# Optimization experiments

Hardware: AMD Instinct MI355X
Metric: run time of the kernel (lower is better)

Reference implementation:

```python
import jax, jax.numpy as jnp
import numpy as np

B = 128
K = 16
# (in_ch, featdim, dim) per stage, matching conv1..conv11
DIMS = [(3, 8, 2048), (8, 32, 1024), (32, 64, 512), (64, 64, 256), (64, 64, 128),
        (64, 128, 64), (128, 256, 32), (256, 512, 16), (512, 512, 8), (512, 512, 4),
        (512, 1024, 2)]


def setup_inputs() -> dict:
    key = jax.random.key(0)
    ks = jax.random.split(key, 64)
    inp = {"x": jax.random.normal(ks[0], (B, 3, 2048), dtype=jnp.float32)}
    i = 1
    for li, (cin, cf, d) in enumerate(DIMS, start=1):
        inp[f"W{li}"] = jax.random.normal(ks[i], (3 * cf, cin), dtype=jnp.float32) / np.sqrt(cin).astype(np.float32); i += 1
        inp[f"b{li}"] = jax.random.normal(ks[i], (3 * cf,), dtype=jnp.float32) * 0.01; i += 1
        inp[f"sel{li}"] = jax.random.randint(ks[i], (d,), 0, 3); i += 1
    inp["fcW"] = jax.random.normal(ks[i], (K, 1024), dtype=jnp.float32) / np.sqrt(1024).astype(np.float32); i += 1
    inp["fcb"] = jax.random.normal(ks[i], (K,), dtype=jnp.float32) * 0.01
    return inp


def kdconv(x, W, b, sel, featdim, dim):
    # 1x1 conv == per-position matmul: x [B, Cin, dim] -> y [B, 3*featdim, dim]
    y = jax.nn.relu(jnp.einsum('oi,bin->bon', W, x) + b[None, :, None])
    y = y.reshape(-1, featdim, 3, dim)
    # kd split-dim gather: pick one of the 3 feature groups per position
    y = jnp.take_along_axis(y, sel[None, None, None, :], axis=2)[:, :, 0, :]  # [B, featdim, dim]
    # pairwise max-pool of sibling leaves
    return y.reshape(-1, featdim, dim // 2, 2).max(axis=-1)  # [B, featdim, dim//2]


def reference(x, sel1, sel2, sel3, sel4, sel5, sel6, sel7, sel8, sel9, sel10, sel11,
              W1, b1, W2, b2, W3, b3, W4, b4, W5, b5, W6, b6, W7, b7, W8, b8,
              W9, b9, W10, b10, W11, b11, fcW, fcb):
    Ws = [W1, W2, W3, W4, W5, W6, W7, W8, W9, W10, W11]
    bs = [b1, b2, b3, b4, b5, b6, b7, b8, b9, b10, b11]
    sels = [sel1, sel2, sel3, sel4, sel5, sel6, sel7, sel8, sel9, sel10, sel11]
    h = x
    for (cin, cf, d), W, b, s in zip(DIMS, Ws, bs, sels):
        h = kdconv(h, W, b, s, cf, d)
    h = h.reshape(-1, 1024)  # [B, 1024]
    return jax.nn.log_softmax(h @ fcW.T + fcb, axis=-1)
```

## Files before the change

kernel.cpp:

```cpp
#include <hip/hip_runtime.h>
#include <math.h>

typedef __attribute__((ext_vector_type(8))) short bf16x8;
typedef __attribute__((ext_vector_type(4))) float f32x4;

__device__ __forceinline__ unsigned short f2bf(float f) {
    unsigned u = __builtin_bit_cast(unsigned, f);
    u += 0x7FFF + ((u >> 16) & 1);
    return (unsigned short)(u >> 16);
}
__device__ __forceinline__ float bf2f(unsigned short h) {
    unsigned u = ((unsigned)h) << 16;
    return __builtin_bit_cast(float, u);
}

#define O_W8 153600
#define O_W9 546816
#define O_W10 1333248
#define O_W11 2119680

__device__ __forceinline__ bf16x8 ldcvt8(const float* p) {
    float4 u0 = *(const float4*)p;
    float4 u1 = *(const float4*)(p + 4);
    bf16x8 r;
    r[0] = (short)f2bf(u0.x); r[1] = (short)f2bf(u0.y);
    r[2] = (short)f2bf(u0.z); r[3] = (short)f2bf(u0.w);
    r[4] = (short)f2bf(u1.x); r[5] = (short)f2bf(u1.y);
    r[6] = (short)f2bf(u1.z); r[7] = (short)f2bf(u1.w);
    return r;
}

template<int CIN>
__device__ __forceinline__ void mfma_tile_f32A(
    const float* a0f, const float* a1f,
    const unsigned short* b0p, const unsigned short* b1p,
    f32x4& acc0, f32x4& acc1)
{
#pragma unroll
    for (int k = 0; k < CIN; k += 32) {
        bf16x8 A0 = ldcvt8(a0f + k);
        bf16x8 A1 = ldcvt8(a1f + k);
        bf16x8 B0 = __builtin_bit_cast(bf16x8, *(const float4*)(const void*)(b0p + k));
        bf16x8 B1 = __builtin_bit_cast(bf16x8, *(const float4*)(const void*)(b1p + k));
        acc0 = __builtin_amdgcn_mfma_f32_16x16x32_bf16(A0, B0, acc0, 0, 0, 0);
        acc1 = __builtin_amdgcn_mfma_f32_16x16x32_bf16(A1, B1, acc1, 0, 0, 0);
    }
}

__device__ __forceinline__ void epilogue_store(
    unsigned short* dst, const f32x4& acc0, const f32x4& acc1,
    const float* bias, int fbase, int s0, int s1)
{
    unsigned short o[4];
#pragma unroll
    for (int r = 0; r < 4; ++r) {
        float v = fmaxf(fmaxf(acc0[r] + bias[(fbase + r) * 3 + s0],
                              acc1[r] + bias[(fbase + r) * 3 + s1]), 0.f);
        o[r] = f2bf(v);
    }
    *(ushort4*)dst = make_ushort4(o[0], o[1], o[2], o[3]);
}

struct FusedParams {
    const float* x;
    const float* W1; const float* B1; const int* S1;
    const float* W2; const float* B2; const int* S2;
    const float* Wsrc[9];
    const float* Bl[9];
    const int*   Sl[9];
    unsigned short* Wb;
    unsigned short* X8;
};

#define A_SELB 0
#define A_XS   8192
#define A_L1O  33536
#define A_WSM  49920
#define A_L2O  53760
#define A_L3O  8192
#define A_L4O  53760
#define A_L5O  8192
#define A_L6O  53760
#define ARENA_BYTES 94720

__global__ __launch_bounds__(1024) void fused17_kernel(FusedParams P)
{
    const int tid = threadIdx.x;

    if (blockIdx.x >= 128) {
        int gt = (blockIdx.x - 128) * 1024 + tid;
        const int we[4] = {393216, 786432, 786432, 1572864};
        const int wo[4] = {O_W8, O_W9, O_W10, O_W11};
#pragma unroll
        for (int li = 0; li < 4; ++li) {
            const float4* src = (const float4*)P.Wsrc[5 + li];
            ushort4* dst = (ushort4*)(P.Wb + wo[li]);
            int n4 = we[li] >> 2;
            for (int i = gt; i < n4; i += 65536) {
                float4 w = src[i];
                dst[i] = make_ushort4(f2bf(w.x), f2bf(w.y), f2bf(w.z), f2bf(w.w));
            }
        }
        return;
    }

    __shared__ __align__(16) char arena[ARENA_BYTES];

    const int bg   = blockIdx.x >> 4;
    const int sl   = blockIdx.x & 15;
    const int lane = tid & 63;
    const int wv   = tid >> 6;
    const int c    = lane & 15, q = lane >> 4;

    int*   si  = (int*)(arena + A_SELB);
    float* bfs = (float*)(arena + A_SELB + 1024);
    const int* S1L = si;
    const int* S2L = si + 128;
    const int* S3L = si + 192;
    const int* S4L = si + 224;
    const int* S5L = si + 240;
    const int* S6L = si + 248;
    const int* S7L = si + 252;
    const float* B3L = bfs;
    const float* B4L = bfs + 192;
    const float* B5L = bfs + 384;
    const float* B6L = bfs + 576;
    const float* B7L = bfs + 960;

    {
        float* xsf = (float*)(arena + A_XS);
        const float* xg = P.x + (size_t)(bg * 16) * 6144 + sl * 128;
        for (int i = tid; i < 6144; i += 1024) {
            int b = i / 384;
            int r = i - b * 384;
            int cc = r >> 7, p = r & 127;
            xsf[b * 396 + cc * 132 + p] = xg[(size_t)b * 6144 + cc * 2048 + p];
        }
        float* wsm = (float*)(arena + A_WSM);
        if (tid < 960) {
            float v;
            if (tid < 72)       v = P.W1[tid];
            else if (tid < 96)  v = P.B1[tid - 72];
            else if (tid < 864) v = P.W2[tid - 96];
            else                v = P.B2[tid - 864];
            wsm[tid] = v;
        }
        if (tid < 128)      si[tid] = P.S1[sl * 128 + tid];
        else if (tid < 192) si[tid] = P.S2[sl * 64 + (tid - 128)];
        else if (tid < 224) si[tid] = P.Sl[0][sl * 32 + (tid - 192)];
        else if (tid < 240) si[tid] = P.Sl[1][sl * 16 + (tid - 224)];
        else if (tid < 248) si[tid] = P.Sl[2][sl * 8  + (tid - 240)];
        else if (tid < 252) si[tid] = P.Sl[3][sl * 4  + (tid - 248)];
        else if (tid < 254) si[tid] = P.Sl[4][sl * 2  + (tid - 252)];
        for (int i = tid; i < 1728; i += 1024) {
            float v;
            if (i < 192)      v = P.Bl[0][i];
            else if (i < 384) v = P.Bl[1][i - 192];
            else if (i < 576) v = P.Bl[2][i - 384];
            else if (i < 960) v = P.Bl[3][i - 576];
            else              v = P.Bl[4][i - 960];
            bfs[i] = v;
        }
    }
    __syncthreads();

    {
        const float* xsf = (const float*)(arena + A_XS);
        const float* wl1 = (const float*)(arena + A_WSM);
        const float* bl1 = wl1 + 72;
        unsigned short* L1o = (unsigned short*)(arena + A_L1O);
        int n = tid >> 4, b = tid & 15;
        int s0 = S1L[2 * n], s1 = S1L[2 * n + 1];
        const float* xb0 = xsf + b * 396 + 2 * n;
        float c0x = xb0[0],   c0y = xb0[1];
        float c1x = xb0[132], c1y = xb0[133];
        float c2x = xb0[264], c2y = xb0[265];
        unsigned short o[8];
#pragma unroll
        for (int f = 0; f < 8; ++f) {
            int r0 = f * 3 + s0, r1 = f * 3 + s1;
            float z0 = fmaf(wl1[r0*3+2], c2x, fmaf(wl1[r0*3+1], c1x, fmaf(wl1[r0*3+0], c0x, bl1[r0])));
            float z1 = fmaf(wl1[r1*3+2], c2y, fmaf(wl1[r1*3+1], c1y, fmaf(wl1[r1*3+0], c0y, bl1[r1])));
            o[f] = f2bf(fmaxf(fmaxf(z0, z1), 0.f));
        }
        unsigned short* dst = L1o + (n * 16 + b) * 8;
        *(ushort4*)dst       = make_ushort4(o[0], o[1], o[2], o[3]);
        *(ushort4*)(dst + 4) = make_ushort4(o[4], o[5], o[6], o[7]);
    }
    __syncthreads();

    {
        const float* wl2 = (const float*)(arena + A_WSM) + 96;
        const float* bl2 = (const float*)(arena + A_WSM) + 864;
        const unsigned short* L1o = (const unsigned short*)(arena + A_L1O);
        unsigned short* L2o = (unsigned short*)(arena + A_L2O);
        int n = tid >> 5, b = (tid >> 1) & 15, fh = tid & 1;
        int s0 = S2L[2 * n], s1 = S2L[2 * n + 1];
        const unsigned short* r0 = L1o + ((2 * n) * 16 + b) * 8;
        const unsigned short* r1 = L1o + ((2 * n + 1) * 16 + b) * 8;
        float xa[8], xb2[8];
        {
            ushort4 u0 = *(const ushort4*)r0, u1 = *(const ushort4*)(r0 + 4);
            ushort4 v0 = *(const ushort4*)r1, v1 = *(const ushort4*)(r1 + 4);
            xa[0]=bf2f(u0.x); xa[1]=bf2f(u0.y); xa[2]=bf2f(u0.z); xa[3]=bf2f(u0.w);
            xa[4]=bf2f(u1.x); xa[5]=bf2f(u1.y); xa[6]=bf2f(u1.z); xa[7]=bf2f(u1.w);
            xb2[0]=bf2f(v0.x); xb2[1]=bf2f(v0.y); xb2[2]=bf2f(v0.z); xb2[3]=bf2f(v0.w);
            xb2[4]=bf2f(v1.x); xb2[5]=bf2f(v1.y); xb2[6]=bf2f(v1.z); xb2[7]=bf2f(v1.w);
        }
        unsigned short o[16];
#pragma unroll
        for (int fl = 0; fl < 16; ++fl) {
            int f = fh * 16 + fl;
            const float* w0 = &wl2[(f * 3 + s0) * 8];
            const float* w1 = &wl2[(f * 3 + s1) * 8];
            float z0 = bl2[f * 3 + s0], z1 = bl2[f * 3 + s1];
#pragma unroll
            for (int k = 0; k < 8; ++k) {
                z0 = fmaf(w0[k], xa[k], z0);
                z1 = fmaf(w1[k], xb2[k], z1);
            }
            o[fl] = f2bf(fmaxf(fmaxf(z0, z1), 0.f));
        }
        unsigned short* dst = L2o + (n * 16 + b) * 40 + fh * 16;
#pragma unroll
        for (int i2 = 0; i2 < 4; ++i2)
            *(ushort4*)(dst + 4 * i2) = make_ushort4(o[4*i2], o[4*i2+1], o[4*i2+2], o[4*i2+3]);
    }
    __syncthreads();

    {
        const unsigned short* L2o = (const unsigned short*)(arena + A_L2O);
        unsigned short* L3o = (unsigned short*)(arena + A_L3O);
        const float* W3f = P.Wsrc[0];
#pragma unroll 2
        for (int t = wv; t < 64; t += 16) {
            int n3 = t >> 2, ft = t & 3;
            int s0 = __builtin_amdgcn_readfirstlane(S3L[2 * n3]);
            int s1 = __builtin_amdgcn_readfirstlane(S3L[2 * n3 + 1]);
            int f0 = ft * 16;
            const float* a0f = W3f + ((f0 + c) * 3 + s0) * 32 + q * 8;
            const float* a1f = W3f + ((f0 + c) * 3 + s1) * 32 + q * 8;
            const unsigned short* bp0 = L2o + ((2 * n3) * 16 + c) * 40 + q * 8;
            const unsigned short* bp1 = L2o + ((2 * n3 + 1) * 16 + c) * 40 + q * 8;
            f32x4 acc0 = {0.f,0.f,0.f,0.f}, acc1 = {0.f,0.f,0.f,0.f};
            mfma_tile_f32A<32>(a0f, a1f, bp0, bp1, acc0, acc1);
            epilogue_store(L3o + (n3 * 16 + c) * 72 + f0 + q * 4,
                           acc0, acc1, B3L, f0 + q * 4, s0, s1);
        }
    }
    __syncthreads();

    {
        const unsigned short* L3o = (const unsigned short*)(arena + A_L3O);
        unsigned short* L4o = (unsigned short*)(arena + A_L4O);
        const float* W4f = P.Wsrc[1];
#pragma unroll
        for (int t = wv; t < 32; t += 16) {
            int n4 = t >> 2, ft = t & 3;
            int s0 = __builtin_amdgcn_readfirstlane(S4L[2 * n4]);
            int s1 = __builtin_amdgcn_readfirstlane(S4L[2 * n4 + 1]);
            int f0 = ft * 16;
            const float* a0f = W4f + ((f0 + c) * 3 + s0) * 64 + q * 8;
            const float* a1f = W4f + ((f0 + c) * 3 + s1) * 64 + q * 8;
            const unsigned short* bp0 = L3o + ((2 * n4) * 16 + c) * 72 + q * 8;
            const unsigned short* bp1 = L3o + ((2 * n4 + 1) * 16 + c) * 72 + q * 8;
            f32x4 acc0 = {0.f,0.f,0.f,0.f}, acc1 = {0.f,0.f,0.f,0.f};
            mfma_tile_f32A<64>(a0f, a1f, bp0, bp1, acc0, acc1);
            epilogue_store(L4o + (n4 * 16 + c) * 72 + f0 + q * 4,
                           acc0, acc1, B4L, f0 + q * 4, s0, s1);
        }
    }
    __syncthreads();

    {
        const unsigned short* L4o = (const unsigned short*)(arena + A_L4O);
        unsigned short* L5o = (unsigned short*)(arena + A_L5O);
        const float* W5f = P.Wsrc[2];
        int t = wv;
        int n5 = t >> 2, ft = t & 3;
        int s0 = __builtin_amdgcn_readfirstlane(S5L[2 * n5]);
        int s1 = __builtin_amdgcn_readfirstlane(S5L[2 * n5 + 1]);
        int f0 = ft * 16;
        const float* a0f = W5f + ((f0 + c) * 3 + s0) * 64 + q * 8;
        const float* a1f = W5f + ((f0 + c) * 3 + s1) * 64 + q * 8;
        const unsigned short* bp0 = L4o + ((2 * n5) * 16 + c) * 72 + q * 8;
        const unsigned short* bp1 = L4o + ((2 * n5 + 1) * 16 + c) * 72 + q * 8;
        f32x4 acc0 = {0.f,0.f,0.f,0.f}, acc1 = {0.f,0.f,0.f,0.f};
        mfma_tile_f32A<64>(a0f, a1f, bp0, bp1, acc0, acc1);
        epilogue_store(L5o + (n5 * 16 + c) * 72 + f0 + q * 4,
                       acc0, acc1, B5L, f0 + q * 4, s0, s1);
    }
    __syncthreads();

    {
        const unsigned short* L5o = (const unsigned short*)(arena + A_L5O);
        unsigned short* L6o = (unsigned short*)(arena + A_L6O);
        const float* W6f = P.Wsrc[3];
        int t = wv;
        int n6 = t >> 3, ft = t & 7;
        int s0 = __builtin_amdgcn_readfirstlane(S6L[2 * n6]);
        int s1 = __builtin_amdgcn_readfirstlane(S6L[2 * n6 + 1]);
        int f0 = ft * 16;
        const float* a0f = W6f + ((f0 + c) * 3 + s0) * 64 + q * 8;
        const float* a1f = W6f + ((f0 + c) * 3 + s1) * 64 + q * 8;
        const unsigned short* bp0 = L5o + ((2 * n6) * 16 + c) * 72 + q * 8;
        const unsigned short* bp1 = L5o + ((2 * n6 + 1) * 16 + c) * 72 + q * 8;
        f32x4 acc0 = {0.f,0.f,0.f,0.f}, acc1 = {0.f,0.f,0.f,0.f};
        mfma_tile_f32A<64>(a0f, a1f, bp0, bp1, acc0, acc1);
        epilogue_store(L6o + (n6 * 16 + c) * 136 + f0 + q * 4,
                       acc0, acc1, B6L, f0 + q * 4, s0, s1);
    }
    __syncthreads();

    {
        const unsigned short* L6o = (const unsigned short*)(arena + A_L6O);
        const float* W7f = P.Wsrc[4];
        int s0 = __builtin_amdgcn_readfirstlane(S7L[0]);
        int s1 = __builtin_amdgcn_readfirstlane(S7L[1]);
        int f0 = wv * 16;
        const float* a0f = W7f + (size_t)((f0 + c) * 3 + s0) * 128 + q * 8;
        const float* a1f = W7f + (size_t)((f0 + c) * 3 + s1) * 128 + q * 8;
        const unsigned short* bp0 = L6o + (0 * 16 + c) * 136 + q * 8;
        const unsigned short* bp1 = L6o + (1 * 16 + c) * 136 + q * 8;
        f32x4 acc0 = {0.f,0.f,0.f,0.f}, acc1 = {0.f,0.f,0.f,0.f};
        mfma_tile_f32A<128>(a0f, a1f, bp0, bp1, acc0, acc1);
        epilogue_store(P.X8 + ((size_t)sl * 128 + bg * 16 + c) * 256 + f0 + q * 4,
                       acc0, acc1, B7L, f0 + q * 4, s0, s1);
    }
}

template<int CIN, int CF, int NP, int MW, int NW>
__global__ __launch_bounds__(256) void mfma_kernel(
    const unsigned short* __restrict__ Xin,
    const unsigned short* __restrict__ Wb,
    const float* __restrict__ bias,
    const int*   __restrict__ sel,
    unsigned short* __restrict__ Xout)
{
    constexpr int FT = CF / (16 * MW);
    constexpr int BT = 128 / (16 * NW);

    const int wid  = threadIdx.x >> 6;
    const int lane = threadIdx.x & 63;
    const int task = blockIdx.x * 4 + wid;
    const int bi = task % BT;
    const int fi = (task / BT) % FT;
    const int n  = task / (BT * FT);

    const int c = lane & 15;
    const int q = lane >> 4;
    const int s0 = __builtin_amdgcn_readfirstlane(sel[2 * n]);
    const int s1 = __builtin_amdgcn_readfirstlane(sel[2 * n + 1]);

    const int f0 = fi * 16 * MW;
    const int b0 = bi * 16 * NW;

    const unsigned short* ap[2][MW];
    const unsigned short* bp[2][NW];
#pragma unroll
    for (int p = 0; p < 2; ++p) {
        int s = p ? s1 : s0;
#pragma unroll
        for (int mi = 0; mi < MW; ++mi)
            ap[p][mi] = Wb + (size_t)((f0 + mi * 16 + c) * 3 + s) * CIN + q * 8;
#pragma unroll
        for (int ni = 0; ni < NW; ++ni)
            bp[p][ni] = Xin + ((size_t)(2 * n + p) * 128 + b0 + ni * 16 + c) * CIN + q * 8;
    }

    f32x4 acc[2][MW][NW];
#pragma unroll
    for (int p = 0; p < 2; ++p)
#pragma unroll
        for (int mi = 0; mi < MW; ++mi)
#pragma unroll
            for (int ni = 0; ni < NW; ++ni)
                acc[p][mi][ni] = (f32x4){0.f, 0.f, 0.f, 0.f};

#pragma unroll 2
    for (int k = 0; k < CIN; k += 32) {
        bf16x8 A[2][MW], B[2][NW];
#pragma unroll
        for (int p = 0; p < 2; ++p) {
#pragma unroll
            for (int mi = 0; mi < MW; ++mi)
                A[p][mi] = __builtin_bit_cast(bf16x8, *(const float4*)(const void*)(ap[p][mi] + k));
#pragma unroll
            for (int ni = 0; ni < NW; ++ni)
                B[p][ni] = __builtin_bit_cast(bf16x8, *(const float4*)(const void*)(bp[p][ni] + k));
        }
#pragma unroll
        for (int p = 0; p < 2; ++p)
#pragma unroll
            for (int mi = 0; mi < MW; ++mi)
#pragma unroll
                for (int ni = 0; ni < NW; ++ni)
                    acc[p][mi][ni] = __builtin_amdgcn_mfma_f32_16x16x32_bf16(
                        A[p][mi], B[p][ni], acc[p][mi][ni], 0, 0, 0);
    }

#pragma unroll
    for (int mi = 0; mi < MW; ++mi) {
        int fbase = f0 + mi * 16 + q * 4;
#pragma unroll
        for (int ni = 0; ni < NW; ++ni) {
            int b = b0 + ni * 16 + c;
            epilogue_store(Xout + ((size_t)n * 128 + b) * CF + fbase,
                           acc[0][mi][ni], acc[1][mi][ni], bias, fbase, s0, s1);
        }
    }
}

__global__ __launch_bounds__(256) void fc_logsoftmax_kernel(
    const unsigned short* __restrict__ h, const float* __restrict__ fcW,
    const float* __restrict__ fcb, float* __restrict__ out)
{
    int b   = blockIdx.x;
    int tid = threadIdx.x;
    int k     = tid & 15;
    int chunk = tid >> 4;

    const float* __restrict__ wk = fcW + (size_t)k * 1024;
    const unsigned short* hb = h + (size_t)b * 1024;

    float partial = 0.0f;
    int j0 = chunk * 64;
#pragma unroll 8
    for (int j = 0; j < 64; ++j)
        partial = fmaf(bf2f(hb[j0 + j]), wk[j0 + j], partial);

    __shared__ float red[16][17];
    red[chunk][k] = partial;
    __syncthreads();

    __shared__ float logits[16];
    if (tid < 16) {
        float s = fcb[tid];
#pragma unroll
        for (int c = 0; c < 16; ++c) s += red[c][tid];
        logits[tid] = s;
    }
    __syncthreads();

    if (tid < 16) {
        float mx = -INFINITY;
#pragma unroll
        for (int kk = 0; kk < 16; ++kk) mx = fmaxf(mx, logits[kk]);
        float se = 0.0f;
#pragma unroll
        for (int kk = 0; kk < 16; ++kk) se += expf(logits[kk] - mx);
        out[b * 16 + tid] = logits[tid] - mx - logf(se);
    }
}

extern "C" void kernel_launch(void* const* d_in, const int* in_sizes, int n_in,
                              void* d_out, int out_size, void* d_ws, size_t ws_size,
                              hipStream_t stream)
{
#define WL(i) (const float*)d_in[1 + 3 * (i)]
#define BL(i) (const float*)d_in[2 + 3 * (i)]
#define SL(i) (const int*)  d_in[3 + 3 * (i)]

    unsigned short* bufA = (unsigned short*)d_ws;
    unsigned short* bufB = bufA + 2u * 1024u * 1024u;
    unsigned short* Wb   = bufB + 2u * 1024u * 1024u;

    FusedParams FP;
    FP.x  = (const float*)d_in[0];
    FP.W1 = WL(0); FP.B1 = BL(0); FP.S1 = SL(0);
    FP.W2 = WL(1); FP.B2 = BL(1); FP.S2 = SL(1);
    for (int i = 0; i < 9; ++i) {
        FP.Wsrc[i] = WL(2 + i);
        FP.Bl[i]   = BL(2 + i);
        FP.Sl[i]   = SL(2 + i);
    }
    FP.Wb = Wb; FP.X8 = bufA;
    fused17_kernel<<<192, 1024, 0, stream>>>(FP);

    mfma_kernel<256, 512, 8, 2, 2><<<128, 256, 0, stream>>>(bufA, Wb + O_W8,  BL(7),  SL(7),  bufB);
    mfma_kernel<512, 512, 4, 1, 1><<<256, 256, 0, stream>>>(bufB, Wb + O_W9,  BL(8),  SL(8),  bufA);
    mfma_kernel<512, 512, 2, 1, 1><<<128, 256, 0, stream>>>(bufA, Wb + O_W10, BL(9),  SL(9),  bufB);
    mfma_kernel<512, 1024, 1, 1, 1><<<128, 256, 0, stream>>>(bufB, Wb + O_W11, BL(10), SL(10), bufA);

    fc_logsoftmax_kernel<<<128, 256, 0, stream>>>(bufA, (const float*)d_in[34], (const float*)d_in[35], (float*)d_out);

#undef WL
#undef BL
#undef SL
}
```

Baseline: 215.0 us.

## Split fused layer 1-7 kernel into L1-2 kernel and L3-7 kernel

The single 1024-thread fused kernel for layers 1-7 is split in two. A 256-thread kernel computes layers 1-2 and packs weights, then writes the layer-2 activations to a global buffer X3. A 512-thread kernel with a smaller shared arena then runs layers 3-7 and reads its input from X3. The aim is to cut per-block shared memory and thread count so occupancy and scheduling improve, at the cost of an extra launch and a global round trip for the layer-2 activations.

New measurement: 220.8 us. 2.7% more time.

```diff
diff --git a/kernel.cpp b/kernel.cpp
--- a/kernel.cpp
+++ b/kernel.cpp
@@ -61,34 +61,21 @@
     *(ushort4*)dst = make_ushort4(o[0], o[1], o[2], o[3]);
 }
 
-struct FusedParams {
+struct KAParams {
     const float* x;
     const float* W1; const float* B1; const int* S1;
     const float* W2; const float* B2; const int* S2;
     const float* Wsrc[9];
-    const float* Bl[9];
-    const int*   Sl[9];
     unsigned short* Wb;
-    unsigned short* X8;
+    unsigned short* X3;
 };
 
-#define A_SELB 0
-#define A_XS   8192
-#define A_L1O  33536
-#define A_WSM  49920
-#define A_L2O  53760
-#define A_L3O  8192
-#define A_L4O  53760
-#define A_L5O  8192
-#define A_L6O  53760
-#define ARENA_BYTES 94720
-
-__global__ __launch_bounds__(1024) void fused17_kernel(FusedParams P)
+__global__ __launch_bounds__(256) void ka_l12_pack(KAParams P)
 {
     const int tid = threadIdx.x;
 
     if (blockIdx.x >= 128) {
-        int gt = (blockIdx.x - 128) * 1024 + tid;
+        int gt = (blockIdx.x - 128) * 256 + tid;
         const int we[4] = {393216, 786432, 786432, 1572864};
         const int wo[4] = {O_W8, O_W9, O_W10, O_W11};
 #pragma unroll
@@ -96,7 +83,7 @@
             const float4* src = (const float4*)P.Wsrc[5 + li];
             ushort4* dst = (ushort4*)(P.Wb + wo[li]);
             int n4 = we[li] >> 2;
-            for (int i = gt; i < n4; i += 65536) {
+            for (int i = gt; i < n4; i += 32768) {
                 float4 w = src[i];
                 dst[i] = make_ushort4(f2bf(w.x), f2bf(w.y), f2bf(w.z), f2bf(w.w));
             }
@@ -104,144 +91,163 @@
         return;
     }
 
-    __shared__ __align__(16) char arena[ARENA_BYTES];
-
+    __shared__ __align__(16) float xsf[16 * 396];
+    __shared__ float wsm[960];
+    __shared__ unsigned short L1o[64 * 16 * 8];
+    __shared__ int selA[192];
+
+    const int bg = blockIdx.x >> 4;
+    const int sl = blockIdx.x & 15;
+
+    {
+        const float* xg = P.x + (size_t)(bg * 16) * 6144 + sl * 128;
+        for (int i = tid; i < 6144; i += 256) {
+            int b = i / 384;
+            int r = i - b * 384;
+            int cc = r >> 7, p = r & 127;
+            xsf[b * 396 + cc * 132 + p] = xg[(size_t)b * 6144 + cc * 2048 + p];
+        }
+        if (tid < 72)            wsm[tid] = P.W1[tid];
+        else if (tid < 96)       wsm[tid] = P.B1[tid - 72];
+        for (int i = tid; i < 768; i += 256) wsm[96 + i] = P.W2[i];
+        if (tid < 96)            wsm[864 + tid] = P.B2[tid];
+        if (tid < 128)           selA[tid] = P.S1[sl * 128 + tid];
+        else if (tid < 192)      selA[tid] = P.S2[sl * 64 + (tid - 128)];
+    }
+    __syncthreads();
+
+    {
+        const float* wl1 = wsm;
+        const float* bl1 = wsm + 72;
+        for (int i = tid; i < 1024; i += 256) {
+            int n = i >> 4, b = i & 15;
+            int s0 = selA[2 * n], s1 = selA[2 * n + 1];
+            const float* xb0 = xsf + b * 396 + 2 * n;
+            float c0x = xb0[0],   c0y = xb0[1];
+            float c1x = xb0[132], c1y = xb0[133];
+            float c2x = xb0[264], c2y = xb0[265];
+            unsigned short o[8];
+#pragma unroll
+            for (int f = 0; f < 8; ++f) {
+                int r0 = f * 3 + s0, r1 = f * 3 + s1;
+                float z0 = fmaf(wl1[r0*3+2], c2x, fmaf(wl1[r0*3+1], c1x, fmaf(wl1[r0*3+0], c0x, bl1[r0])));
+                float z1 = fmaf(wl1[r1*3+2], c2y, fmaf(wl1[r1*3+1], c1y, fmaf(wl1[r1*3+0], c0y, bl1[r1])));
+                o[f] = f2bf(fmaxf(fmaxf(z0, z1), 0.f));
+            }
+            unsigned short* dst = L1o + (n * 16 + b) * 8;
+            *(ushort4*)dst       = make_ushort4(o[0], o[1], o[2], o[3]);
+            *(ushort4*)(dst + 4) = make_ushort4(o[4], o[5], o[6], o[7]);
+        }
+    }
+    __syncthreads();
+
+    {
+        const float* wl2 = wsm + 96;
+        const float* bl2 = wsm + 864;
+        for (int i = tid; i < 1024; i += 256) {
+            int n = i >> 5, b = (i >> 1) & 15, fh = i & 1;
+            int s0 = selA[128 + 2 * n], s1 = selA[128 + 2 * n + 1];
+            const unsigned short* r0 = L1o + ((2 * n) * 16 + b) * 8;
+            const unsigned short* r1 = L1o + ((2 * n + 1) * 16 + b) * 8;
+            float xa[8], xb2[8];
+            {
+                ushort4 u0 = *(const ushort4*)r0, u1 = *(const ushort4*)(r0 + 4);
+                ushort4 v0 = *(const ushort4*)r1, v1 = *(const ushort4*)(r1 + 4);
+                xa[0]=bf2f(u0.x); xa[1]=bf2f(u0.y); xa[2]=bf2f(u0.z); xa[3]=bf2f(u0.w);
+                xa[4]=bf2f(u1.x); xa[5]=bf2f(u1.y); xa[6]=bf2f(u1.z); xa[7]=bf2f(u1.w);
+                xb2[0]=bf2f(v0.x); xb2[1]=bf2f(v0.y); xb2[2]=bf2f(v0.z); xb2[3]=bf2f(v0.w);
+                xb2[4]=bf2f(v1.x); xb2[5]=bf2f(v1.y); xb2[6]=bf2f(v1.z); xb2[7]=bf2f(v1.w);
+            }
+            unsigned short o[16];
+#pragma unroll
+            for (int fl = 0; fl < 16; ++fl) {
+                int f = fh * 16 + fl;
+                const float* w0 = &wl2[(f * 3 + s0) * 8];
+                const float* w1 = &wl2[(f * 3 + s1) * 8];
+                float z0 = bl2[f * 3 + s0], z1 = bl2[f * 3 + s1];
+#pragma unroll
+                for (int k = 0; k < 8; ++k) {
+                    z0 = fmaf(w0[k], xa[k], z0);
+                    z1 = fmaf(w1[k], xb2[k], z1);
+                }
+                o[fl] = f2bf(fmaxf(fmaxf(z0, z1), 0.f));
+            }
+            unsigned short* dst = P.X3 + ((size_t)(sl * 32 + n) * 128 + bg * 16 + b) * 32 + fh * 16;
+#pragma unroll
+            for (int i2 = 0; i2 < 4; ++i2)
+                *(ushort4*)(dst + 4 * i2) = make_ushort4(o[4*i2], o[4*i2+1], o[4*i2+2], o[4*i2+3]);
+        }
+    }
+}
+
+struct KBParams {
+    const float* Wsrc[9];
+    const float* Bl[9];
+    const int*   Sl[9];
+    const unsigned short* X3;
+    unsigned short* X8;
+};
+
+#define B_SELB 0
+#define B_L3O  8192
+#define B_L4O  45056
+#define B_L5O  8192
+#define B_L6O  45056
+#define B_ARENA 63488
+
+__global__ __launch_bounds__(512) void kb_l37(KBParams P)
+{
+    __shared__ __align__(16) char arena[B_ARENA];
+
+    const int tid  = threadIdx.x;
     const int bg   = blockIdx.x >> 4;
     const int sl   = blockIdx.x & 15;
     const int lane = tid & 63;
     const int wv   = tid >> 6;
     const int c    = lane & 15, q = lane >> 4;
 
-    int*   si  = (int*)(arena + A_SELB);
-    float* bfs = (float*)(arena + A_SELB + 1024);
-    const int* S1L = si;
-    const int* S2L = si + 128;
-    const int* S3L = si + 192;
-    const int* S4L = si + 224;
-    const int* S5L = si + 240;
-    const int* S6L = si + 248;
-    const int* S7L = si + 252;
+    int*   si  = (int*)(arena + B_SELB);
+    float* bfs = (float*)(arena + B_SELB + 1024);
+    const int* S3L = si;
+    const int* S4L = si + 32;
+    const int* S5L = si + 48;
+    const int* S6L = si + 56;
+    const int* S7L = si + 60;
     const float* B3L = bfs;
     const float* B4L = bfs + 192;
     const float* B5L = bfs + 384;
     const float* B6L = bfs + 576;
     const float* B7L = bfs + 960;
 
-    {
-        float* xsf = (float*)(arena + A_XS);
-        const float* xg = P.x + (size_t)(bg * 16) * 6144 + sl * 128;
-        for (int i = tid; i < 6144; i += 1024) {
-            int b = i / 384;
-            int r = i - b * 384;
-            int cc = r >> 7, p = r & 127;
-            xsf[b * 396 + cc * 132 + p] = xg[(size_t)b * 6144 + cc * 2048 + p];
-        }
-        float* wsm = (float*)(arena + A_WSM);
-        if (tid < 960) {
-            float v;
-            if (tid < 72)       v = P.W1[tid];
-            else if (tid < 96)  v = P.B1[tid - 72];
-            else if (tid < 864) v = P.W2[tid - 96];
-            else                v = P.B2[tid - 864];
-            wsm[tid] = v;
-        }
-        if (tid < 128)      si[tid] = P.S1[sl * 128 + tid];
-        else if (tid < 192) si[tid] = P.S2[sl * 64 + (tid - 128)];
-        else if (tid < 224) si[tid] = P.Sl[0][sl * 32 + (tid - 192)];
-        else if (tid < 240) si[tid] = P.Sl[1][sl * 16 + (tid - 224)];
-        else if (tid < 248) si[tid] = P.Sl[2][sl * 8  + (tid - 240)];
-        else if (tid < 252) si[tid] = P.Sl[3][sl * 4  + (tid - 248)];
-        else if (tid < 254) si[tid] = P.Sl[4][sl * 2  + (tid - 252)];
-        for (int i = tid; i < 1728; i += 1024) {
-            float v;
-            if (i < 192)      v = P.Bl[0][i];
-            else if (i < 384) v = P.Bl[1][i - 192];
-            else if (i < 576) v = P.Bl[2][i - 384];
-            else if (i < 960) v = P.Bl[3][i - 576];
-            else              v = P.Bl[4][i - 960];
-            bfs[i] = v;
-        }
-    }
-    __syncthreads();
-
-    {
-        const float* xsf = (const float*)(arena + A_XS);
-        const float* wl1 = (const float*)(arena + A_WSM);
-        const float* bl1 = wl1 + 72;
-        unsigned short* L1o = (unsigned short*)(arena + A_L1O);
-        int n = tid >> 4, b = tid & 15;
-        int s0 = S1L[2 * n], s1 = S1L[2 * n + 1];
-        const float* xb0 = xsf + b * 396 + 2 * n;
-        float c0x = xb0[0],   c0y = xb0[1];
-        float c1x = xb0[132], c1y = xb0[133];
-        float c2x = xb0[264], c2y = xb0[265];
-        unsigned short o[8];
-#pragma unroll
-        for (int f = 0; f < 8; ++f) {
-            int r0 = f * 3 + s0, r1 = f * 3 + s1;
-            float z0 = fmaf(wl1[r0*3+2], c2x, fmaf(wl1[r0*3+1], c1x, fmaf(wl1[r0*3+0], c0x, bl1[r0])));
-            float z1 = fmaf(wl1[r1*3+2], c2y, fmaf(wl1[r1*3+1], c1y, fmaf(wl1[r1*3+0], c0y, bl1[r1])));
-            o[f] = f2bf(fmaxf(fmaxf(z0, z1), 0.f));
-        }
-        unsigned short* dst = L1o + (n * 16 + b) * 8;
-        *(ushort4*)dst       = make_ushort4(o[0], o[1], o[2], o[3]);
-        *(ushort4*)(dst + 4) = make_ushort4(o[4], o[5], o[6], o[7]);
-    }
-    __syncthreads();
-
-    {
-        const float* wl2 = (const float*)(arena + A_WSM) + 96;
-        const float* bl2 = (const float*)(arena + A_WSM) + 864;
-        const unsigned short* L1o = (const unsigned short*)(arena + A_L1O);
-        unsigned short* L2o = (unsigned short*)(arena + A_L2O);
-        int n = tid >> 5, b = (tid >> 1) & 15, fh = tid & 1;
-        int s0 = S2L[2 * n], s1 = S2L[2 * n + 1];
-        const unsigned short* r0 = L1o + ((2 * n) * 16 + b) * 8;
-        const unsigned short* r1 = L1o + ((2 * n + 1) * 16 + b) * 8;
-        float xa[8], xb2[8];
-        {
-            ushort4 u0 = *(const ushort4*)r0, u1 = *(const ushort4*)(r0 + 4);
-            ushort4 v0 = *(const ushort4*)r1, v1 = *(const ushort4*)(r1 + 4);
-            xa[0]=bf2f(u0.x); xa[1]=bf2f(u0.y); xa[2]=bf2f(u0.z); xa[3]=bf2f(u0.w);
-            xa[4]=bf2f(u1.x); xa[5]=bf2f(u1.y); xa[6]=bf2f(u1.z); xa[7]=bf2f(u1.w);
-            xb2[0]=bf2f(v0.x); xb2[1]=bf2f(v0.y); xb2[2]=bf2f(v0.z); xb2[3]=bf2f(v0.w);
-            xb2[4]=bf2f(v1.x); xb2[5]=bf2f(v1.y); xb2[6]=bf2f(v1.z); xb2[7]=bf2f(v1.w);
-        }
-        unsigned short o[16];
-#pragma unroll
-        for (int fl = 0; fl < 16; ++fl) {
-            int f = fh * 16 + fl;
-            const float* w0 = &wl2[(f * 3 + s0) * 8];
-            const float* w1 = &wl2[(f * 3 + s1) * 8];
-            float z0 = bl2[f * 3 + s0], z1 = bl2[f * 3 + s1];
-#pragma unroll
-            for (int k = 0; k < 8; ++k) {
-                z0 = fmaf(w0[k], xa[k], z0);
-                z1 = fmaf(w1[k], xb2[k], z1);
-            }
-            o[fl] = f2bf(fmaxf(fmaxf(z0, z1), 0.f));
-        }
-        unsigned short* dst = L2o + (n * 16 + b) * 40 + fh * 16;
-#pragma unroll
-        for (int i2 = 0; i2 < 4; ++i2)
-            *(ushort4*)(dst + 4 * i2) = make_ushort4(o[4*i2], o[4*i2+1], o[4*i2+2], o[4*i2+3]);
-    }
-    __syncthreads();
-
-    {
-        const unsigned short* L2o = (const unsigned short*)(arena + A_L2O);
-        unsigned short* L3o = (unsigned short*)(arena + A_L3O);
+    if (tid < 32)       si[tid] = P.Sl[0][sl * 32 + tid];
+    else if (tid < 48)  si[tid] = P.Sl[1][sl * 16 + (tid - 32)];
+    else if (tid < 56)  si[tid] = P.Sl[2][sl * 8 + (tid - 48)];
+    else if (tid < 60)  si[tid] = P.Sl[3][sl * 4 + (tid - 56)];
+    else if (tid < 62)  si[tid] = P.Sl[4][sl * 2 + (tid - 60)];
+    for (int i = tid; i < 1728; i += 512) {
+        float v;
+        if (i < 192)      v = P.Bl[0][i];
+        else if (i < 384) v = P.Bl[1][i - 192];
+        else if (i < 576) v = P.Bl[2][i - 384];
+        else if (i < 960) v = P.Bl[3][i - 576];
+        else              v = P.Bl[4][i - 960];
+        bfs[i] = v;
+    }
+    __syncthreads();
+
+    {
+        unsigned short* L3o = (unsigned short*)(arena + B_L3O);
         const float* W3f = P.Wsrc[0];
 #pragma unroll 2
-        for (int t = wv; t < 64; t += 16) {
+        for (int t = wv; t < 64; t += 8) {
             int n3 = t >> 2, ft = t & 3;
             int s0 = __builtin_amdgcn_readfirstlane(S3L[2 * n3]);
             int s1 = __builtin_amdgcn_readfirstlane(S3L[2 * n3 + 1]);
             int f0 = ft * 16;
             const float* a0f = W3f + ((f0 + c) * 3 + s0) * 32 + q * 8;
             const float* a1f = W3f + ((f0 + c) * 3 + s1) * 32 + q * 8;
-            const unsigned short* bp0 = L2o + ((2 * n3) * 16 + c) * 40 + q * 8;
-            const unsigned short* bp1 = L2o + ((2 * n3 + 1) * 16 + c) * 40 + q * 8;
+            const unsigned short* bp0 = P.X3 + ((size_t)(sl * 32 + 2 * n3) * 128 + bg * 16 + c) * 32 + q * 8;
+            const unsigned short* bp1 = P.X3 + ((size_t)(sl * 32 + 2 * n3 + 1) * 128 + bg * 16 + c) * 32 + q * 8;
             f32x4 acc0 = {0.f,0.f,0.f,0.f}, acc1 = {0.f,0.f,0.f,0.f};
             mfma_tile_f32A<32>(a0f, a1f, bp0, bp1, acc0, acc1);
             epilogue_store(L3o + (n3 * 16 + c) * 72 + f0 + q * 4,
@@ -251,11 +257,11 @@
     __syncthreads();
 
     {
-        const unsigned short* L3o = (const unsigned short*)(arena + A_L3O);
-        unsigned short* L4o = (unsigned short*)(arena + A_L4O);
+        const unsigned short* L3o = (const unsigned short*)(arena + B_L3O);
+        unsigned short* L4o = (unsigned short*)(arena + B_L4O);
         const float* W4f = P.Wsrc[1];
-#pragma unroll
-        for (int t = wv; t < 32; t += 16) {
+#pragma unroll 2
+        for (int t = wv; t < 32; t += 8) {
             int n4 = t >> 2, ft = t & 3;
             int s0 = __builtin_amdgcn_readfirstlane(S4L[2 * n4]);
             int s1 = __builtin_amdgcn_readfirstlane(S4L[2 * n4 + 1]);
@@ -273,59 +279,66 @@
     __syncthreads();
 
     {
-        const unsigned short* L4o = (const unsigned short*)(arena + A_L4O);
-        unsigned short* L5o = (unsigned short*)(arena + A_L5O);
+        const unsigned short* L4o = (const unsigned short*)(arena + B_L4O);
+        unsigned short* L5o = (unsigned short*)(arena + B_L5O);
         const float* W5f = P.Wsrc[2];
-        int t = wv;
-        int n5 = t >> 2, ft = t & 3;
-        int s0 = __builtin_amdgcn_readfirstlane(S5L[2 * n5]);
-        int s1 = __builtin_amdgcn_readfirstlane(S5L[2 * n5 + 1]);
-        int f0 = ft * 16;
-        const float* a0f = W5f + ((f0 + c) * 3 + s0) * 64 + q * 8;
-        const float* a1f = W5f + ((f0 + c) * 3 + s1) * 64 + q * 8;
-        const unsigned short* bp0 = L4o + ((2 * n5) * 16 + c) * 72 + q * 8;
-        const unsigned short* bp1 = L4o + ((2 * n5 + 1) * 16 + c) * 72 + q * 8;
-        f32x4 acc0 = {0.f,0.f,0.f,0.f}, acc1 = {0.f,0.f,0.f,0.f};
-        mfma_tile_f32A<64>(a0f, a1f, bp0, bp1, acc0, acc1);
-        epilogue_store(L5o + (n5 * 16 + c) * 72 + f0 + q * 4,
-                       acc0, acc1, B5L, f0 + q * 4, s0, s1);
-    }
-    __syncthreads();
-
-    {
-        const unsigned short* L5o = (const unsigned short*)(arena + A_L5O);
-        unsigned short* L6o = (unsigned short*)(arena + A_L6O);
+#pragma unroll
+        for (int t = wv; t < 16; t += 8) {
+            int n5 = t >> 2, ft = t & 3;
+            int s0 = __builtin_amdgcn_readfirstlane(S5L[2 * n5]);
+            int s1 = __builtin_amdgcn_readfirstlane(S5L[2 * n5 + 1]);
+            int f0 = ft * 16;
+            const float* a0f = W5f + ((f0 + c) * 3 + s0) * 64 + q * 8;
+            const float* a1f = W5f + ((f0 + c) * 3 + s1) * 64 + q * 8;
+            const unsigned short* bp0 = L4o + ((2 * n5) * 16 + c) * 72 + q * 8;
+            const unsigned short* bp1 = L4o + ((2 * n5 + 1) * 16 + c) * 72 + q * 8;
+            f32x4 acc0 = {0.f,0.f,0.f,0.f}, acc1 = {0.f,0.f,0.f,0.f};
+            mfma_tile_f32A<64>(a0f, a1f, bp0, bp1, acc0, acc1);
+            epilogue_store(L5o + (n5 * 16 + c) * 72 + f0 + q * 4,
+                           acc0, acc1, B5L, f0 + q * 4, s0, s1);
+        }
+    }
+    __syncthreads();
+
+    {
+        const unsigned short* L5o = (const unsigned short*)(arena + B_L5O);
+        unsigned short* L6o = (unsigned short*)(arena + B_L6O);
         const float* W6f = P.Wsrc[3];
-        int t = wv;
-        int n6 = t >> 3, ft = t & 7;
-        int s0 = __builtin_amdgcn_readfirstlane(S6L[2 * n6]);
-        int s1 = __builtin_amdgcn_readfirstlane(S6L[2 * n6 + 1]);
-        int f0 = ft * 16;
-        const float* a0f = W6f + ((f0 + c) * 3 + s0) * 64 + q * 8;
-        const float* a1f = W6f + ((f0 + c) * 3 + s1) * 64 + q * 8;
-        const unsigned short* bp0 = L5o + ((2 * n6) * 16 + c) * 72 + q * 8;
-        const unsigned short* bp1 = L5o + ((2 * n6 + 1) * 16 + c) * 72 + q * 8;
-        f32x4 acc0 = {0.f,0.f,0.f,0.f}, acc1 = {0.f,0.f,0.f,0.f};
-        mfma_tile_f32A<64>(a0f, a1f, bp0, bp1, acc0, acc1);
-        epilogue_store(L6o + (n6 * 16 + c) * 136 + f0 + q * 4,
-                       acc0, acc1, B6L, f0 + q * 4, s0, s1);
-    }
-    __syncthreads();
-
-    {
-        const unsigned short* L6o = (const unsigned short*)(arena + A_L6O);
+#pragma unroll
+        for (int t = wv; t < 16; t += 8) {
+            int n6 = t >> 3, ft = t & 7;
+            int s0 = __builtin_amdgcn_readfirstlane(S6L[2 * n6]);
+            int s1 = __builtin_amdgcn_readfirstlane(S6L[2 * n6 + 1]);
+            int f0 = ft * 16;
+            const float* a0f = W6f + ((f0 + c) * 3 + s0) * 64 + q * 8;
+            const float* a1f = W6f + ((f0 + c) * 3 + s1) * 64 + q * 8;
+            const unsigned short* bp0 = L5o + ((2 * n6) * 16 + c) * 72 + q * 8;
+            const unsigned short* bp1 = L5o + ((2 * n6 + 1) * 16 + c) * 72 + q * 8;
+            f32x4 acc0 = {0.f,0.f,0.f,0.f}, acc1 = {0.f,0.f,0.f,0.f};
+            mfma_tile_f32A<64>(a0f, a1f, bp0, bp1, acc0, acc1);
+            epilogue_store(L6o + (n6 * 16 + c) * 136 + f0 + q * 4,
+                           acc0, acc1, B6L, f0 + q * 4, s0, s1);
+        }
+    }
+    __syncthreads();
+
+    {
+        const unsigned short* L6o = (const unsigned short*)(arena + B_L6O);
         const float* W7f = P.Wsrc[4];
         int s0 = __builtin_amdgcn_readfirstlane(S7L[0]);
         int s1 = __builtin_amdgcn_readfirstlane(S7L[1]);
-        int f0 = wv * 16;
-        const float* a0f = W7f + (size_t)((f0 + c) * 3 + s0) * 128 + q * 8;
-        const float* a1f = W7f + (size_t)((f0 + c) * 3 + s1) * 128 + q * 8;
-        const unsigned short* bp0 = L6o + (0 * 16 + c) * 136 + q * 8;
-        const unsigned short* bp1 = L6o + (1 * 16 + c) * 136 + q * 8;
-        f32x4 acc0 = {0.f,0.f,0.f,0.f}, acc1 = {0.f,0.f,0.f,0.f};
-        mfma_tile_f32A<128>(a0f, a1f, bp0, bp1, acc0, acc1);
-        epilogue_store(P.X8 + ((size_t)sl * 128 + bg * 16 + c) * 256 + f0 + q * 4,
-                       acc0, acc1, B7L, f0 + q * 4, s0, s1);
+#pragma unroll
+        for (int t = wv; t < 16; t += 8) {
+            int f0 = t * 16;
+            const float* a0f = W7f + (size_t)((f0 + c) * 3 + s0) * 128 + q * 8;
+            const float* a1f = W7f + (size_t)((f0 + c) * 3 + s1) * 128 + q * 8;
+            const unsigned short* bp0 = L6o + (0 * 16 + c) * 136 + q * 8;
+            const unsigned short* bp1 = L6o + (1 * 16 + c) * 136 + q * 8;
+            f32x4 acc0 = {0.f,0.f,0.f,0.f}, acc1 = {0.f,0.f,0.f,0.f};
+            mfma_tile_f32A<128>(a0f, a1f, bp0, bp1, acc0, acc1);
+            epilogue_store(P.X8 + ((size_t)sl * 128 + bg * 16 + c) * 256 + f0 + q * 4,
+                           acc0, acc1, B7L, f0 + q * 4, s0, s1);
+        }
     }
 }
 
@@ -463,19 +476,25 @@
 
     unsigned short* bufA = (unsigned short*)d_ws;
     unsigned short* bufB = bufA + 2u * 1024u * 1024u;
-    unsigned short* Wb   = bufB + 2u * 1024u * 1024u;
-
-    FusedParams FP;
-    FP.x  = (const float*)d_in[0];
-    FP.W1 = WL(0); FP.B1 = BL(0); FP.S1 = SL(0);
-    FP.W2 = WL(1); FP.B2 = BL(1); FP.S2 = SL(1);
+    unsigned short* X3   = bufB + 2u * 1024u * 1024u;
+    unsigned short* Wb   = X3   + 2u * 1024u * 1024u;
+
+    KAParams KA;
+    KA.x  = (const float*)d_in[0];
+    KA.W1 = WL(0); KA.B1 = BL(0); KA.S1 = SL(0);
+    KA.W2 = WL(1); KA.B2 = BL(1); KA.S2 = SL(1);
+    for (int i = 0; i < 9; ++i) KA.Wsrc[i] = WL(2 + i);
+    KA.Wb = Wb; KA.X3 = X3;
+    ka_l12_pack<<<256, 256, 0, stream>>>(KA);
+
+    KBParams KB;
     for (int i = 0; i < 9; ++i) {
-        FP.Wsrc[i] = WL(2 + i);
-        FP.Bl[i]   = BL(2 + i);
-        FP.Sl[i]   = SL(2 + i);
-    }
-    FP.Wb = Wb; FP.X8 = bufA;
-    fused17_kernel<<<192, 1024, 0, stream>>>(FP);
+        KB.Wsrc[i] = WL(2 + i);
+        KB.Bl[i]   = BL(2 + i);
+        KB.Sl[i]   = SL(2 + i);
+    }
+    KB.X3 = X3; KB.X8 = bufA;
+    kb_l37<<<128, 512, 0, stream>>>(KB);
 
     mfma_kernel<256, 512, 8, 2, 2><<<128, 256, 0, stream>>>(bufA, Wb + O_W8,  BL(7),  SL(7),  bufB);
     mfma_kernel<512, 512, 4, 1, 1><<<256, 256, 0, stream>>>(bufB, Wb + O_W9,  BL(8),  SL(8),  bufA);
```
